# Kernel optimization log

Hardware: AMD Instinct MI355X
Metric: run time of the kernel (lower is better)

## Reference

```python
import jax, jax.numpy as jnp
import numpy as np

NC = 80          # num classes (len(yolov8.names))
CONF = 0.25      # ultralytics conf_thres default
IOU_T = 0.45     # ultralytics iou_thres default
MAX_DET = 300    # module default max_det
K = 1024         # pre-NMS candidate cap (static stand-in for max_nms)
MAX_WH = 7680.0  # ultralytics class-offset for multi-class NMS


def setup_inputs() -> dict:
    key = jax.random.key(0)
    k1, k2, k3 = jax.random.split(key, 3)
    B, A = 32, 8400
    # YOLOv8 head layout: rows 0:4 = xywh (pixels), rows 4: = sigmoid class scores
    xy = jax.random.uniform(k1, (B, 2, A), dtype=jnp.float32) * 640.0
    wh = jax.random.uniform(k2, (B, 2, A), dtype=jnp.float32) * 160.0 + 8.0
    scores = jax.random.uniform(k3, (B, NC, A), dtype=jnp.float32) ** 3  # mostly below conf_thres
    preds = jnp.concatenate([xy, wh, scores], axis=1)  # [B, 4+NC, A]
    return {"preds": preds}


def _box_iou(b):
    # b: [K, 4] xyxy -> [K, K] pairwise IoU
    area = (b[:, 2] - b[:, 0]) * (b[:, 3] - b[:, 1])
    lt = jnp.maximum(b[:, None, :2], b[None, :, :2])
    rb = jnp.minimum(b[:, None, 2:], b[None, :, 2:])
    wh = jnp.clip(rb - lt, 0.0)
    inter = wh[..., 0] * wh[..., 1]
    return inter / (area[:, None] + area[None, :] - inter + 1e-7)


def _nms_single(pred):
    # pred: [4+NC, A]
    boxes_xywh = pred[:4].T           # [A, 4]
    cls_scores = pred[4:].T           # [A, NC]
    conf = cls_scores.max(-1)         # best-class confidence per anchor
    cls = jnp.argmax(cls_scores, -1)
    score = jnp.where(conf > CONF, conf, 0.0)
    top, idx = jax.lax.top_k(score, K)            # K candidates by confidence
    xywh = boxes_xywh[idx]
    half = xywh[:, 2:] * 0.5
    boxes = jnp.concatenate([xywh[:, :2] - half, xywh[:, :2] + half], -1)  # xyxy
    cls_k = cls[idx]
    valid = top > CONF
    # multi-class NMS via per-class coordinate offset (ultralytics trick)
    iou = _box_iou(boxes + (cls_k.astype(boxes.dtype) * MAX_WH)[:, None])
    ar = jnp.arange(K)

    def body(i, st):
        supp, keep = st
        ki = valid[i] & ~supp[i]
        keep = keep.at[i].set(ki)
        supp = supp | (ki & (iou[i] > IOU_T) & (ar > i))
        return supp, keep

    _, keep = jax.lax.fori_loop(0, K, body,
                                (jnp.zeros(K, bool), jnp.zeros(K, bool)))
    fscore = jnp.where(keep, top, 0.0)
    sc, order = jax.lax.top_k(fscore, MAX_DET)
    det = jnp.concatenate(
        [boxes[order], top[order][:, None], cls_k[order].astype(boxes.dtype)[:, None]], -1)
    # pad invalid rows with value NC in every column (matches F.pad(value=len(names)))
    return jnp.where((sc > CONF)[:, None], det, jnp.float32(NC))


def reference(preds):
    # [B, MAX_DET, 6] -> (x1, y1, x2, y2, conf, cls), padded rows filled with NC
    return jax.vmap(_nms_single)(preds)
```

## Files before the change

### kernel.cpp

```cpp
#include <hip/hip_runtime.h>
#include <stdint.h>

typedef unsigned long long u64;
typedef unsigned int u32;

#define NC 80
#define CONF_T 0.25f
#define IOU_THR 0.45f
#define MAX_DET 300
#define KBIG 1024
#define A_ANCH 8400
#define NROWS 84
#define MAX_WH 7680.0f
#define HBINS 256
#define BIN_BASE 0x3e80u

__device__ __forceinline__ void hadd(u32* h, u32 bin, bool m, int lane) {
    u64 act = __ballot(m);
    if (act == 0) return;
    int fl = __ffsll((unsigned long long)act) - 1;
    u32 fb = __shfl(bin, fl);
    u64 same = __ballot(m && (bin == fb));
    if (lane == fl) atomicAdd(&h[fb], (u32)__popcll(same));
    if (m && (bin != fb)) atomicAdd(&h[bin], 1u);
}

__global__ __launch_bounds__(256) void yolo_conf_kernel(const float* __restrict__ preds,
                                                        u64* __restrict__ keys,
                                                        float4* __restrict__ obox,
                                                        u32* __restrict__ hist) {
    __shared__ u32 lh[HBINS];
    const int lane = threadIdx.x & 63;
    int b = blockIdx.x / 9;
    int g = (blockIdx.x % 9) * 256 + threadIdx.x;
    lh[threadIdx.x] = 0;
    __syncthreads();

    if (g < A_ANCH / 4) {
        int a0 = g * 4;
        const float* base = preds + ((size_t)b * NROWS + 4) * A_ANCH + a0;
        float4 best = *(const float4*)base;
        int bcx = 0, bcy = 0, bcz = 0, bcw = 0;
#pragma unroll 4
        for (int c = 1; c < NC; ++c) {
            float4 v = *(const float4*)(base + (size_t)c * A_ANCH);
            if (v.x > best.x) { best.x = v.x; bcx = c; }
            if (v.y > best.y) { best.y = v.y; bcy = c; }
            if (v.z > best.z) { best.z = v.z; bcz = c; }
            if (v.w > best.w) { best.w = v.w; bcw = c; }
        }
        float sc[4] = {(best.x > CONF_T) ? best.x : 0.0f, (best.y > CONF_T) ? best.y : 0.0f,
                       (best.z > CONF_T) ? best.z : 0.0f, (best.w > CONF_T) ? best.w : 0.0f};
        int cl[4] = {bcx, bcy, bcz, bcw};
        u64* ko = keys + (size_t)b * A_ANCH + a0;
        ulonglong2 k01, k23;
        k01.x = ((u64)__float_as_uint(sc[0]) << 32) | ((u64)(16383 - a0) << 7) | (u64)cl[0];
        k01.y = ((u64)__float_as_uint(sc[1]) << 32) | ((u64)(16383 - (a0 + 1)) << 7) | (u64)cl[1];
        k23.x = ((u64)__float_as_uint(sc[2]) << 32) | ((u64)(16383 - (a0 + 2)) << 7) | (u64)cl[2];
        k23.y = ((u64)__float_as_uint(sc[3]) << 32) | ((u64)(16383 - (a0 + 3)) << 7) | (u64)cl[3];
        *(ulonglong2*)ko = k01;
        *(ulonglong2*)(ko + 2) = k23;

        const float* pb = preds + (size_t)b * NROWS * A_ANCH + a0;
        float4 xv = *(const float4*)(pb);
        float4 yv = *(const float4*)(pb + A_ANCH);
        float4 wv = *(const float4*)(pb + 2 * A_ANCH);
        float4 hv = *(const float4*)(pb + 3 * A_ANCH);
        float xs[4] = {xv.x, xv.y, xv.z, xv.w};
        float ys[4] = {yv.x, yv.y, yv.z, yv.w};
        float ws[4] = {wv.x, wv.y, wv.z, wv.w};
        float hs[4] = {hv.x, hv.y, hv.z, hv.w};
#pragma unroll
        for (int q = 0; q < 4; ++q) {
            float hw = __fmul_rn(ws[q], 0.5f), hh = __fmul_rn(hs[q], 0.5f);
            float x1 = __fsub_rn(xs[q], hw), x2 = __fadd_rn(xs[q], hw);
            float y1 = __fsub_rn(ys[q], hh), y2 = __fadd_rn(ys[q], hh);
            float off = __fmul_rn((float)cl[q], MAX_WH);
            float4 ob;
            ob.x = __fadd_rn(x1, off); ob.y = __fadd_rn(y1, off);
            ob.z = __fadd_rn(x2, off); ob.w = __fadd_rn(y2, off);
            obox[(size_t)b * A_ANCH + a0 + q] = ob;
            u32 sb = __float_as_uint(sc[q]);
            u32 bin = (sb >> 16) - BIN_BASE;
            if (bin > 255u) bin = 255u;
            hadd(lh, bin, sb != 0u, lane);
        }
    }
    __syncthreads();
    u32 c = lh[threadIdx.x];
    if (c) atomicAdd(&hist[(size_t)b * HBINS + threadIdx.x], c);
}

__device__ __forceinline__ float iou_f(float ix1, float iy1, float ix2, float iy2, float iar,
                                       float jx1, float jy1, float jx2, float jy2, float jar) {
    float lx = fmaxf(ix1, jx1), ly = fmaxf(iy1, jy1);
    float rx = fminf(ix2, jx2), ry = fminf(iy2, jy2);
    float ww = fmaxf(__fsub_rn(rx, lx), 0.0f);
    float hh = fmaxf(__fsub_rn(ry, ly), 0.0f);
    float inter = __fmul_rn(ww, hh);
    float den = __fadd_rn(__fsub_rn(__fadd_rn(iar, jar), inter), 1e-7f);
    return __fdiv_rn(inter, den);
}

__device__ __forceinline__ u64 bstep(u64 v, u32 idx, u32 size, u32 stride) {
    u64 v2 = __shfl_xor((unsigned long long)v, (int)stride, 64);
    bool keep_big = (((idx & stride) == 0) == ((idx & size) == 0));
    return ((v > v2) == keep_big) ? v : v2;
}

__device__ __forceinline__ void radix_scan(u32* hist, int nb, int shift, u32* s_scal,
                                           u32* wsum, int tid, int lane, int wid) {
    int per = nb >> 10; if (per == 0) per = 1;
    int na = nb / per;
    u32 rem = s_scal[1];
    u32 Pk = s_scal[0];
    int hi = nb - 1 - per * tid;
    u32 s = 0;
    if (tid < na)
        for (int q = 0; q < per; ++q) s += hist[hi - q];
    u32 pre = s;
#pragma unroll
    for (int off = 1; off < 64; off <<= 1) {
        u32 o = __shfl_up(pre, off);
        if (lane >= off) pre += o;
    }
    if (lane == 63) wsum[wid] = pre;
    __syncthreads();
    u32 base = 0;
    for (int w = 0; w < wid; ++w) base += wsum[w];
    u32 run = base + pre - s;
    if (tid < na) {
        for (int q = 0; q < per; ++q) {
            int d = hi - q;
            u32 g = hist[d];
            if (run < rem && rem <= run + g) {
                s_scal[0] = Pk | ((u32)d << shift);
                s_scal[1] = rem - run;
            }
            run += g;
        }
    }
    __syncthreads();
}

union U2 {
    u32 hist[4096];
    struct { u32 eqw[264]; u32 wpre[264]; } tie;
};

__global__ __launch_bounds__(1024) void yolo_nms_kernel(const float* __restrict__ preds,
                                                        const u64* __restrict__ keys,
                                                        const float4* __restrict__ obox,
                                                        const u32* __restrict__ hist,
                                                        float* __restrict__ out) {
    const int b = blockIdx.x;
    const int tid = threadIdx.x;
    const int lane = tid & 63;
    const int wid = tid >> 6;

    __shared__ U2 u2;
    __shared__ u64 skey[KBIG];
    __shared__ float BX1[KBIG], BY1[KBIG], BX2[KBIG], BY2[KBIG], BAR[KBIG];
    __shared__ int keptlist[364];
    __shared__ float kx1[364], ky1[364], kx2[364], ky2[364], kar[364];
    __shared__ u32 kcls[364];
    __shared__ u64 rows[64];
    __shared__ u32 wsum[16];
    __shared__ u32 s_scal[4];
    __shared__ u32 s_cnt;
    __shared__ u32 s_csupp[2];
    __shared__ u32 s_nkept;

    const u64* kb = keys + (size_t)b * A_ANCH;

    u32 vals[9];
#pragma unroll
    for (int it = 0; it < 9; ++it) {
        int a = tid + it * 1024;
        vals[it] = (a < A_ANCH) ? (u32)(kb[a] >> 32) : 0u;
    }

    const u32* hb = hist + (size_t)b * HBINS;
    {
        u32 g = (tid < HBINS) ? hb[HBINS - 1 - tid] : 0u;
        u32 pre = g;
#pragma unroll
        for (int off = 1; off < 64; off <<= 1) {
            u32 o = __shfl_up(pre, off);
            if (lane >= off) pre += o;
        }
        if (lane == 63) wsum[wid] = pre;
        __syncthreads();
        u32 base = 0;
        for (int w = 0; w < wid; ++w) base += wsum[w];
        pre += base;
        u32 run = pre - g;
        if (tid < HBINS) {
            if (run < 512u && 512u <= pre) { s_scal[0] = (u32)(HBINS - 1 - tid); s_scal[2] = pre; }
            if (tid == HBINS - 1) {
                s_scal[3] = pre;
                if (pre < 512u) { s_scal[0] = 0; s_scal[2] = pre; }
            }
        }
        __syncthreads();
    }
    const u32 Pbin16 = BIN_BASE + s_scal[0];
    const u32 Cfast = s_scal[2];
    const u32 validN = s_scal[3];

    for (int pass = 0; pass < 2; ++pass) {
        u32 Ccand;
        if (pass == 0) {
            if (Cfast > (u32)KBIG) continue;
            Ccand = Cfast;
            skey[tid] = 0;
            if (tid == 0) { s_cnt = 0; s_nkept = 0; s_csupp[0] = 0; s_csupp[1] = 0; }
            __syncthreads();
#pragma unroll
            for (int it = 0; it < 9; ++it) {
                int a = tid + it * 1024;
                u32 v = vals[it];
                bool take = (a < A_ANCH) && (v != 0u) && ((v >> 16) >= Pbin16);
                u64 m = __ballot(take);
                if (m) {
                    int fl = __ffsll((unsigned long long)m) - 1;
                    u32 basep = 0;
                    if (lane == fl) basep = atomicAdd(&s_cnt, (u32)__popcll(m));
                    basep = __shfl(basep, fl);
                    if (take) {
                        u32 pos = basep + (u32)__popcll(m & ((1ull << lane) - 1ull));
                        if (pos < (u32)KBIG) skey[pos] = kb[a];
                    }
                }
            }
            __syncthreads();
        } else {
            for (int i = tid; i < 4096; i += 1024) u2.hist[i] = 0;
            if (tid == 0) {
                s_scal[0] = 0; s_scal[1] = (u32)KBIG; s_scal[2] = 0;
                s_nkept = 0; s_csupp[0] = 0; s_csupp[1] = 0;
            }
            __syncthreads();
#pragma unroll
            for (int it = 0; it < 9; ++it) {
                int a = tid + it * 1024;
                hadd(u2.hist, vals[it] >> 20, a < A_ANCH, lane);
            }
            __syncthreads();
            radix_scan(u2.hist, 4096, 20, s_scal, wsum, tid, lane, wid);
            for (int i = tid; i < 4096; i += 1024) u2.hist[i] = 0;
            __syncthreads();
            u32 Pk = s_scal[0];
#pragma unroll
            for (int it = 0; it < 9; ++it) {
                int a = tid + it * 1024;
                u32 v = vals[it];
                bool m = (a < A_ANCH) && ((v & 0xFFF00000u) == Pk);
                hadd(u2.hist, (v >> 8) & 4095u, m, lane);
            }
            __syncthreads();
            radix_scan(u2.hist, 4096, 8, s_scal, wsum, tid, lane, wid);
            for (int i = tid; i < 256; i += 1024) u2.hist[i] = 0;
            __syncthreads();
            Pk = s_scal[0];
#pragma unroll
            for (int it = 0; it < 9; ++it) {
                int a = tid + it * 1024;
                u32 v = vals[it];
                bool m = (a < A_ANCH) && ((v & 0xFFFFFF00u) == Pk);
                hadd(u2.hist, v & 255u, m, lane);
            }
            __syncthreads();
            radix_scan(u2.hist, 256, 0, s_scal, wsum, tid, lane, wid);
            const u32 P = s_scal[0];
            const u32 tEq = s_scal[1];
            if (tid < 264) u2.tie.eqw[tid] = 0;
            __syncthreads();
#pragma unroll
            for (int it = 0; it < 9; ++it) {
                int a = tid + it * 1024;
                if (a < A_ANCH && vals[it] == P) atomicOr(&u2.tie.eqw[a >> 5], 1u << (a & 31));
            }
            __syncthreads();
            if (wid == 0) {
                u32 cw[5], loc = 0;
#pragma unroll
                for (int q = 0; q < 5; ++q) {
                    int w2 = lane * 5 + q;
                    u32 e = (w2 < 264) ? u2.tie.eqw[w2] : 0u;
                    cw[q] = (u32)__popc(e); loc += cw[q];
                }
                u32 pre = loc;
#pragma unroll
                for (int off = 1; off < 64; off <<= 1) {
                    u32 o = __shfl_up(pre, off);
                    if (lane >= off) pre += o;
                }
                u32 run = pre - loc;
#pragma unroll
                for (int q = 0; q < 5; ++q) {
                    int w2 = lane * 5 + q;
                    if (w2 < 264) u2.tie.wpre[w2] = run;
                    run += cw[q];
                }
            }
            __syncthreads();
#pragma unroll
            for (int it = 0; it < 9; ++it) {
                int a = tid + it * 1024;
                bool take = false;
                if (a < A_ANCH) {
                    u32 v = vals[it];
                    take = v > P;
                    if (!take && v == P) {
                        u32 r = u2.tie.wpre[a >> 5] +
                                (u32)__popc(u2.tie.eqw[a >> 5] & ((1u << (a & 31)) - 1u));
                        take = (r < tEq);
                    }
                }
                u64 m = __ballot(take);
                if (m) {
                    int fl = __ffsll((unsigned long long)m) - 1;
                    u32 basep = 0;
                    if (lane == fl) basep = atomicAdd(&s_scal[2], (u32)__popcll(m));
                    basep = __shfl(basep, fl);
                    if (take) {
                        u32 pos = basep + (u32)__popcll(m & ((1ull << lane) - 1ull));
                        if (pos < (u32)KBIG) skey[pos] = kb[a];
                    }
                }
            }
            __syncthreads();
            Ccand = KBIG;
        }

        {
            u64 v = skey[tid];
#pragma unroll
            for (u32 size = 2; size <= 64; size <<= 1)
#pragma unroll
                for (u32 stride = size >> 1; stride >= 1; stride >>= 1)
                    v = bstep(v, (u32)tid, size, stride);
            for (u32 size = 128; size <= 1024; size <<= 1) {
                for (u32 stride = size >> 1; stride >= 64; stride >>= 1) {
                    skey[tid] = v;
                    __syncthreads();
                    u64 v2 = skey[tid ^ stride];
                    bool keep_big = ((((u32)tid & stride) == 0) == (((u32)tid & size) == 0));
                    v = ((v > v2) == keep_big) ? v : v2;
                    __syncthreads();
                }
#pragma unroll
                for (u32 stride = 32; stride >= 1; stride >>= 1)
                    v = bstep(v, (u32)tid, size, stride);
            }
            skey[tid] = v;
            __syncthreads();
        }

        {
            u64 key = skey[tid];
            int idx = 16383 - (int)((key >> 7) & 16383u);
            if (idx >= A_ANCH || idx < 0) idx = 0;
            float4 ob = obox[(size_t)b * A_ANCH + idx];
            BX1[tid] = ob.x; BY1[tid] = ob.y; BX2[tid] = ob.z; BY2[tid] = ob.w;
            BAR[tid] = __fmul_rn(__fsub_rn(ob.z, ob.x), __fsub_rn(ob.w, ob.y));
        }
        __syncthreads();

        const int nchunks = (int)((Ccand + 63u) >> 6);
        for (int c = 0; c < nchunks; ++c) {
            int j = c * 64 + lane;
            u64 keyj = skey[j];
            float scj = __uint_as_float((u32)(keyj >> 32));
            u32 clsj = (u32)(keyj & 127u);
            float jx1 = BX1[j], jy1 = BY1[j], jx2 = BX2[j], jy2 = BY2[j], jar = BAR[j];

            u32 nk = s_nkept;
            bool suppbit = false;
            for (u32 k = wid; k < nk; k += 16) {
                bool cm = (kcls[k] == clsj);
                if (__ballot(cm)) {
                    float iou = iou_f(kx1[k], ky1[k], kx2[k], ky2[k], kar[k],
                                      jx1, jy1, jx2, jy2, jar);
                    suppbit |= (cm && (iou > IOU_THR));
                }
            }
            u64 bm = __ballot(suppbit);
            if (bm && lane == 0) {
                atomicOr(&s_csupp[0], (u32)bm);
                atomicOr(&s_csupp[1], (u32)(bm >> 32));
            }
#pragma unroll
            for (int p2 = 0; p2 < 4; ++p2) {
                int i = p2 * 16 + wid;
                int ci = c * 64 + i;
                u32 clsi = (u32)(skey[ci] & 127u);
                u64 m = 0;
                if (__ballot(clsi == clsj)) {
                    float iou = iou_f(BX1[ci], BY1[ci], BX2[ci], BY2[ci], BAR[ci],
                                      jx1, jy1, jx2, jy2, jar);
                    m = __ballot((lane > i) && (iou > IOU_THR));
                }
                if (lane == 0) rows[i] = m;
            }
            __syncthreads();
            if (wid == 0) {
                u64 row = rows[lane];
                u32 rlo = (u32)row, rhi = (u32)(row >> 32);
                u64 csupp = (((u64)s_csupp[1]) << 32) | (u64)s_csupp[0];
                u64 validm = __ballot(scj > CONF_T) & ~csupp;
                u64 supp = 0, keep = 0;
#pragma unroll
                for (int i = 0; i < 64; ++i) {
                    u64 ri = (((u64)(u32)__builtin_amdgcn_readlane((int)rhi, i)) << 32) |
                             (u64)(u32)__builtin_amdgcn_readlane((int)rlo, i);
                    bool ki = (((validm & ~supp) >> i) & 1ull) != 0;
                    if (ki) { keep |= (1ull << i); supp |= ri; }
                }
                u32 basek = s_nkept;
                if ((keep >> lane) & 1ull) {
                    u32 slot = basek + (u32)__popcll(keep & ((1ull << lane) - 1ull));
                    keptlist[slot] = j;
                    kx1[slot] = jx1; ky1[slot] = jy1;
                    kx2[slot] = jx2; ky2[slot] = jy2;
                    kar[slot] = jar; kcls[slot] = clsj;
                }
                if (lane == 0) {
                    s_nkept = basek + (u32)__popcll(keep);
                    s_csupp[0] = 0; s_csupp[1] = 0;
                }
            }
            __syncthreads();
            if (s_nkept >= MAX_DET) break;
        }

        u32 nk = s_nkept;
        bool finished = (nk >= MAX_DET) || (Ccand >= validN) || (pass == 1);
        if (!finished) continue;

        if (tid < MAX_DET) {
            float row[6];
            int t = (tid < (int)(nk < MAX_DET ? nk : MAX_DET)) ? keptlist[tid] : -1;
            if (t >= 0) {
                u64 key = skey[t];
                float score = __uint_as_float((u32)(key >> 32));
                int cls = (int)(key & 127u);
                int idx = 16383 - (int)((key >> 7) & 16383u);
                const float* pb = preds + (size_t)b * NROWS * A_ANCH + idx;
                float x = pb[0], y = pb[A_ANCH], w = pb[2 * A_ANCH], h = pb[3 * A_ANCH];
                float hw = __fmul_rn(w, 0.5f), hh = __fmul_rn(h, 0.5f);
                row[0] = __fsub_rn(x, hw);
                row[1] = __fsub_rn(y, hh);
                row[2] = __fadd_rn(x, hw);
                row[3] = __fadd_rn(y, hh);
                row[4] = score;
                row[5] = (float)cls;
            } else {
                row[0] = row[1] = row[2] = row[3] = row[4] = row[5] = (float)NC;
            }
            float* o = out + ((size_t)b * MAX_DET + tid) * 6;
#pragma unroll
            for (int q = 0; q < 6; ++q) o[q] = row[q];
        }
        break;
    }
}

extern "C" void kernel_launch(void* const* d_in, const int* in_sizes, int n_in,
                              void* d_out, int out_size, void* d_ws, size_t ws_size,
                              hipStream_t stream) {
    const float* preds = (const float*)d_in[0];
    float* out = (float*)d_out;
    int B = in_sizes[0] / (NROWS * A_ANCH);
    u64* keys = (u64*)d_ws;
    float4* obox = (float4*)(keys + (size_t)B * A_ANCH);
    u32* hist = (u32*)(obox + (size_t)B * A_ANCH);
    (void)hipMemsetAsync(hist, 0, (size_t)B * HBINS * sizeof(u32), stream);
    yolo_conf_kernel<<<dim3(B * 9), dim3(256), 0, stream>>>(preds, keys, obox, hist);
    yolo_nms_kernel<<<dim3(B), dim3(1024), 0, stream>>>(preds, keys, obox, hist, out);
}
```

Measured before the change: 78.49 us.

## Move histogram and box decode into NMS kernel, drop obox buffer and memset

The confidence kernel now writes only the packed score/index/class keys, processing two anchors per thread with 512-thread blocks. The per-batch score histogram is rebuilt in shared memory inside the NMS kernel from the key values it already loads. Candidate boxes are decoded from preds on demand for the 1024 selected anchors instead of being stored for all anchors. This removes the memset launch, the global histogram atomics and the full obox write/read traffic. In exchange the NMS kernel, which runs one block per batch, takes on extra histogram work and scattered gathers from preds.

```diff
diff --git a/kernel.cpp b/kernel.cpp
--- a/kernel.cpp
+++ b/kernel.cpp
@@ -15,80 +15,27 @@
 #define HBINS 256
 #define BIN_BASE 0x3e80u
 
-__device__ __forceinline__ void hadd(u32* h, u32 bin, bool m, int lane) {
-    u64 act = __ballot(m);
-    if (act == 0) return;
-    int fl = __ffsll((unsigned long long)act) - 1;
-    u32 fb = __shfl(bin, fl);
-    u64 same = __ballot(m && (bin == fb));
-    if (lane == fl) atomicAdd(&h[fb], (u32)__popcll(same));
-    if (m && (bin != fb)) atomicAdd(&h[bin], 1u);
-}
-
-__global__ __launch_bounds__(256) void yolo_conf_kernel(const float* __restrict__ preds,
-                                                        u64* __restrict__ keys,
-                                                        float4* __restrict__ obox,
-                                                        u32* __restrict__ hist) {
-    __shared__ u32 lh[HBINS];
-    const int lane = threadIdx.x & 63;
+__global__ __launch_bounds__(512) void yolo_conf_kernel(const float* __restrict__ preds,
+                                                        u64* __restrict__ keys) {
     int b = blockIdx.x / 9;
-    int g = (blockIdx.x % 9) * 256 + threadIdx.x;
-    lh[threadIdx.x] = 0;
-    __syncthreads();
-
-    if (g < A_ANCH / 4) {
-        int a0 = g * 4;
-        const float* base = preds + ((size_t)b * NROWS + 4) * A_ANCH + a0;
-        float4 best = *(const float4*)base;
-        int bcx = 0, bcy = 0, bcz = 0, bcw = 0;
-#pragma unroll 4
-        for (int c = 1; c < NC; ++c) {
-            float4 v = *(const float4*)(base + (size_t)c * A_ANCH);
-            if (v.x > best.x) { best.x = v.x; bcx = c; }
-            if (v.y > best.y) { best.y = v.y; bcy = c; }
-            if (v.z > best.z) { best.z = v.z; bcz = c; }
-            if (v.w > best.w) { best.w = v.w; bcw = c; }
-        }
-        float sc[4] = {(best.x > CONF_T) ? best.x : 0.0f, (best.y > CONF_T) ? best.y : 0.0f,
-                       (best.z > CONF_T) ? best.z : 0.0f, (best.w > CONF_T) ? best.w : 0.0f};
-        int cl[4] = {bcx, bcy, bcz, bcw};
-        u64* ko = keys + (size_t)b * A_ANCH + a0;
-        ulonglong2 k01, k23;
-        k01.x = ((u64)__float_as_uint(sc[0]) << 32) | ((u64)(16383 - a0) << 7) | (u64)cl[0];
-        k01.y = ((u64)__float_as_uint(sc[1]) << 32) | ((u64)(16383 - (a0 + 1)) << 7) | (u64)cl[1];
-        k23.x = ((u64)__float_as_uint(sc[2]) << 32) | ((u64)(16383 - (a0 + 2)) << 7) | (u64)cl[2];
-        k23.y = ((u64)__float_as_uint(sc[3]) << 32) | ((u64)(16383 - (a0 + 3)) << 7) | (u64)cl[3];
-        *(ulonglong2*)ko = k01;
-        *(ulonglong2*)(ko + 2) = k23;
-
-        const float* pb = preds + (size_t)b * NROWS * A_ANCH + a0;
-        float4 xv = *(const float4*)(pb);
-        float4 yv = *(const float4*)(pb + A_ANCH);
-        float4 wv = *(const float4*)(pb + 2 * A_ANCH);
-        float4 hv = *(const float4*)(pb + 3 * A_ANCH);
-        float xs[4] = {xv.x, xv.y, xv.z, xv.w};
-        float ys[4] = {yv.x, yv.y, yv.z, yv.w};
-        float ws[4] = {wv.x, wv.y, wv.z, wv.w};
-        float hs[4] = {hv.x, hv.y, hv.z, hv.w};
-#pragma unroll
-        for (int q = 0; q < 4; ++q) {
-            float hw = __fmul_rn(ws[q], 0.5f), hh = __fmul_rn(hs[q], 0.5f);
-            float x1 = __fsub_rn(xs[q], hw), x2 = __fadd_rn(xs[q], hw);
-            float y1 = __fsub_rn(ys[q], hh), y2 = __fadd_rn(ys[q], hh);
-            float off = __fmul_rn((float)cl[q], MAX_WH);
-            float4 ob;
-            ob.x = __fadd_rn(x1, off); ob.y = __fadd_rn(y1, off);
-            ob.z = __fadd_rn(x2, off); ob.w = __fadd_rn(y2, off);
-            obox[(size_t)b * A_ANCH + a0 + q] = ob;
-            u32 sb = __float_as_uint(sc[q]);
-            u32 bin = (sb >> 16) - BIN_BASE;
-            if (bin > 255u) bin = 255u;
-            hadd(lh, bin, sb != 0u, lane);
-        }
-    }
-    __syncthreads();
-    u32 c = lh[threadIdx.x];
-    if (c) atomicAdd(&hist[(size_t)b * HBINS + threadIdx.x], c);
+    int g = (blockIdx.x % 9) * 512 + threadIdx.x;
+    if (g >= A_ANCH / 2) return;
+    int a0 = g * 2;
+    const float* base = preds + ((size_t)b * NROWS + 4) * A_ANCH + a0;
+    float2 best = *(const float2*)base;
+    int bc0 = 0, bc1 = 0;
+#pragma unroll 8
+    for (int c = 1; c < NC; ++c) {
+        float2 v = *(const float2*)(base + (size_t)c * A_ANCH);
+        if (v.x > best.x) { best.x = v.x; bc0 = c; }
+        if (v.y > best.y) { best.y = v.y; bc1 = c; }
+    }
+    float s0 = (best.x > CONF_T) ? best.x : 0.0f;
+    float s1 = (best.y > CONF_T) ? best.y : 0.0f;
+    ulonglong2 kk;
+    kk.x = ((u64)__float_as_uint(s0) << 32) | ((u64)(16383 - a0) << 7) | (u64)bc0;
+    kk.y = ((u64)__float_as_uint(s1) << 32) | ((u64)(16383 - (a0 + 1)) << 7) | (u64)bc1;
+    *(ulonglong2*)(keys + (size_t)b * A_ANCH + a0) = kk;
 }
 
 __device__ __forceinline__ float iou_f(float ix1, float iy1, float ix2, float iy2, float iar,
@@ -100,6 +47,16 @@
     float inter = __fmul_rn(ww, hh);
     float den = __fadd_rn(__fsub_rn(__fadd_rn(iar, jar), inter), 1e-7f);
     return __fdiv_rn(inter, den);
+}
+
+__device__ __forceinline__ void hadd(u32* h, u32 bin, bool m, int lane) {
+    u64 act = __ballot(m);
+    if (act == 0) return;
+    int fl = __ffsll((unsigned long long)act) - 1;
+    u32 fb = __shfl(bin, fl);
+    u64 same = __ballot(m && (bin == fb));
+    if (lane == fl) atomicAdd(&h[fb], (u32)__popcll(same));
+    if (m && (bin != fb)) atomicAdd(&h[bin], 1u);
 }
 
 __device__ __forceinline__ u64 bstep(u64 v, u32 idx, u32 size, u32 stride) {
@@ -150,8 +107,6 @@
 
 __global__ __launch_bounds__(1024) void yolo_nms_kernel(const float* __restrict__ preds,
                                                         const u64* __restrict__ keys,
-                                                        const float4* __restrict__ obox,
-                                                        const u32* __restrict__ hist,
                                                         float* __restrict__ out) {
     const int b = blockIdx.x;
     const int tid = threadIdx.x;
@@ -180,9 +135,20 @@
         vals[it] = (a < A_ANCH) ? (u32)(kb[a] >> 32) : 0u;
     }
 
-    const u32* hb = hist + (size_t)b * HBINS;
+    if (tid < HBINS) u2.hist[tid] = 0;
+    __syncthreads();
+#pragma unroll
+    for (int it = 0; it < 9; ++it) {
+        int a = tid + it * 1024;
+        u32 v = vals[it];
+        u32 bin = (v >> 16) - BIN_BASE;
+        if (bin > 255u) bin = 255u;
+        hadd(u2.hist, bin, (a < A_ANCH) && (v != 0u), lane);
+    }
+    __syncthreads();
+
     {
-        u32 g = (tid < HBINS) ? hb[HBINS - 1 - tid] : 0u;
+        u32 g = (tid < HBINS) ? u2.hist[HBINS - 1 - tid] : 0u;
         u32 pre = g;
 #pragma unroll
         for (int off = 1; off < 64; off <<= 1) {
@@ -360,11 +326,22 @@
 
         {
             u64 key = skey[tid];
+            int cls = (int)(key & 127u);
             int idx = 16383 - (int)((key >> 7) & 16383u);
             if (idx >= A_ANCH || idx < 0) idx = 0;
-            float4 ob = obox[(size_t)b * A_ANCH + idx];
-            BX1[tid] = ob.x; BY1[tid] = ob.y; BX2[tid] = ob.z; BY2[tid] = ob.w;
-            BAR[tid] = __fmul_rn(__fsub_rn(ob.z, ob.x), __fsub_rn(ob.w, ob.y));
+            const float* pb = preds + (size_t)b * NROWS * A_ANCH + idx;
+            float x = pb[0];
+            float y = pb[A_ANCH];
+            float w = pb[2 * A_ANCH];
+            float h = pb[3 * A_ANCH];
+            float hw = __fmul_rn(w, 0.5f), hh = __fmul_rn(h, 0.5f);
+            float x1 = __fsub_rn(x, hw), x2 = __fadd_rn(x, hw);
+            float y1 = __fsub_rn(y, hh), y2 = __fadd_rn(y, hh);
+            float off = __fmul_rn((float)cls, MAX_WH);
+            float bx1 = __fadd_rn(x1, off), bx2 = __fadd_rn(x2, off);
+            float by1 = __fadd_rn(y1, off), by2 = __fadd_rn(y2, off);
+            BX1[tid] = bx1; BY1[tid] = by1; BX2[tid] = bx2; BY2[tid] = by2;
+            BAR[tid] = __fmul_rn(__fsub_rn(bx2, bx1), __fsub_rn(by2, by1));
         }
         __syncthreads();
 
@@ -472,11 +449,8 @@
                               hipStream_t stream) {
     const float* preds = (const float*)d_in[0];
     float* out = (float*)d_out;
+    u64* keys = (u64*)d_ws;
     int B = in_sizes[0] / (NROWS * A_ANCH);
-    u64* keys = (u64*)d_ws;
-    float4* obox = (float4*)(keys + (size_t)B * A_ANCH);
-    u32* hist = (u32*)(obox + (size_t)B * A_ANCH);
-    (void)hipMemsetAsync(hist, 0, (size_t)B * HBINS * sizeof(u32), stream);
-    yolo_conf_kernel<<<dim3(B * 9), dim3(256), 0, stream>>>(preds, keys, obox, hist);
-    yolo_nms_kernel<<<dim3(B), dim3(1024), 0, stream>>>(preds, keys, obox, hist, out);
-}
+    yolo_conf_kernel<<<dim3(B * 9), dim3(512), 0, stream>>>(preds, keys);
+    yolo_nms_kernel<<<dim3(B), dim3(1024), 0, stream>>>(preds, keys, out);
+}
```

New measurement: 68.28 us. 1.15x faster.
